# Kernel tuning notes

Hardware: AMD Instinct MI355X
Metric: run time of the kernel (lower is better)

Reference implementation:

```python
import jax, jax.numpy as jnp
import numpy as np

D_MODEL = 1024
D_STATE = 128
HEADDIM = 64
EXPAND = 2
CHUNK = 64
D_CONV = 4
D_INNER = EXPAND * D_MODEL          # 2048
NHEADS = D_INNER // HEADDIM         # 32
D_IN_PROJ = 2 * D_INNER + 2 * D_STATE + NHEADS  # 4384
CONV_CH = D_INNER + 2 * D_STATE     # 2304
EPS = 1e-5


def segsum(x):
    # x: (..., T) -> (..., T, T); out[i, j] = sum_{k=j+1..i} x[k] for i>=j else -inf
    T = x.shape[-1]
    m1 = jnp.tril(jnp.ones((T, T), bool), -1)
    xr = jnp.where(m1, x[..., :, None], 0.0)   # zero above/at diagonal before cumsum
    s = jnp.cumsum(xr, axis=-2)
    m0 = jnp.tril(jnp.ones((T, T), bool), 0)
    return jnp.where(m0, s, -jnp.inf)


def ssd(x, A, B, C, chunk):
    # x: (b, L, h, p); A: (b, L, h); B, C: (b, L, n)  (the h=1 dim of the torch code is squeezed)
    b, L, h, p = x.shape
    c = L // chunk
    x = x.reshape(b, c, chunk, h, p)
    A = A.reshape(b, c, chunk, h).transpose(0, 3, 1, 2)  # (b, h, c, l)
    B = B.reshape(b, c, chunk, -1)                       # (b, c, l, n)
    C = C.reshape(b, c, chunk, -1)
    A_cum = jnp.cumsum(A, axis=-1)                       # (b, h, c, l)
    Lm = jnp.exp(segsum(A))                              # (b, h, c, l, l)
    # intra-chunk (diagonal block) output
    Y_diag = jnp.einsum('bcln,bcsn,bhcls,bcshp->bclhp', C, B, Lm, x)
    # per-chunk states
    decay_states = jnp.exp(A_cum[:, :, :, -1:] - A_cum)  # (b, h, c, l)
    states = jnp.einsum('bcln,bhcl,bclhp->bchpn', B, decay_states, x)
    init = jnp.zeros_like(states[:, :1])
    states = jnp.concatenate([init, states], axis=1)     # (b, c+1, h, p, n)
    # inter-chunk recurrence
    Ac_last = jnp.pad(A_cum[:, :, :, -1], ((0, 0), (0, 0), (1, 0)))  # (b, h, c+1)
    decay_chunk = jnp.exp(segsum(Ac_last))               # (b, h, c+1, c+1)
    new_states = jnp.einsum('bhzc,bchpn->bzhpn', decay_chunk, states)
    states = new_states[:, :-1]                          # (b, c, h, p, n)
    sdo = jnp.exp(A_cum)
    Y_off = jnp.einsum('bcln,bchpn,bhcl->bclhp', C, states, sdo)
    return (Y_diag + Y_off).reshape(b, L, h, p)


def setup_inputs() -> dict:
    key = jax.random.key(0)
    ks = jax.random.split(key, 8)
    return {
        'u': jax.random.normal(ks[0], (2, 4096, D_MODEL), jnp.float32),
        'W_in': jax.random.normal(ks[1], (D_MODEL, D_IN_PROJ), jnp.float32) * 0.02,
        'conv_w': jax.random.normal(ks[2], (CONV_CH, D_CONV), jnp.float32) * 0.3,
        'conv_b': jax.random.normal(ks[3], (CONV_CH,), jnp.float32) * 0.1,
        'dt_bias': jax.random.normal(ks[4], (NHEADS,), jnp.float32),
        'A_log': jax.random.normal(ks[5], (NHEADS,), jnp.float32) * 0.5,
        'D': jax.random.normal(ks[6], (NHEADS,), jnp.float32),
        'norm_w': jnp.ones((D_INNER,), jnp.float32),
        'W_out': jax.random.normal(ks[7], (D_INNER, D_MODEL), jnp.float32) * 0.02,
    }


def reference(u, W_in, conv_w, conv_b, dt_bias, A_log, D, norm_w, W_out):
    b, L, _ = u.shape
    zxbcdt = u @ W_in                                    # (b, L, 4384)
    z = zxbcdt[..., :D_INNER]
    xBC = zxbcdt[..., D_INNER:D_INNER + CONV_CH]
    dt = jax.nn.softplus(zxbcdt[..., -NHEADS:] + dt_bias)  # (b, L, h)
    # depthwise causal conv (Conv1d pad=d_conv-1, truncated to L == left-pad only)
    xc = jnp.pad(xBC.transpose(0, 2, 1), ((0, 0), (0, 0), (D_CONV - 1, 0)))
    xc = jax.lax.conv_general_dilated(
        xc, conv_w[:, None, :], (1,), 'VALID',
        feature_group_count=CONV_CH,
        dimension_numbers=('NCH', 'OIH', 'NCH')) + conv_b[None, :, None]
    xBC = jax.nn.silu(xc.transpose(0, 2, 1))             # (b, L, 2304)
    x = xBC[..., :D_INNER].reshape(b, L, NHEADS, HEADDIM)
    B = xBC[..., D_INNER:D_INNER + D_STATE]
    C = xBC[..., D_INNER + D_STATE:]
    A = -jnp.exp(A_log)                                  # (h,)
    y = ssd(x * dt[..., None], A * dt, B, C, CHUNK)
    y = y + x * D[:, None]
    y = y.reshape(b, L, D_INNER)
    # RMSNorm with gate z
    y = y * jax.nn.silu(z)
    y = y * jax.lax.rsqrt(jnp.mean(y * y, axis=-1, keepdims=True) + EPS) * norm_w
    return y @ W_out
```

## Files before the change

### kernel.cpp

```cpp
#include <hip/hip_runtime.h>
#include <hip/hip_bf16.h>
#include <math.h>

#define D_MODEL   1024
#define D_STATE   128
#define HEADDIM   64
#define CHUNK     64
#define D_INNER   2048
#define NHEADS    32
#define D_IN_PROJ 4384
#define CONV_CH   2304
#define RCOLS     2336
#define WINT_ROWS 4480
#define BATCH     2
#define SEQ       4096
#define NCHUNK    64
#define ROWS      (BATCH*SEQ)
#define EPS_RMS   1e-5f

typedef __hip_bfloat16 bf16;
typedef __bf16 bf16x8_t __attribute__((ext_vector_type(8)));
typedef float  f32x4_t  __attribute__((ext_vector_type(4)));

__device__ __forceinline__ float siluf_(float x){ return x/(1.f+expf(-x)); }
__device__ __forceinline__ void  stf(float* p, float v){ *p = v; }
__device__ __forceinline__ void  stf(bf16* p, float v){ *p = __float2bfloat16(v); }

__device__ __forceinline__ __bf16 tobf(float v){
    __hip_bfloat16 t = __float2bfloat16(v);
    return *reinterpret_cast<__bf16*>(&t);
}
__device__ __forceinline__ unsigned short bfbits(float v){
    __hip_bfloat16 t = __float2bfloat16(v);
    return *reinterpret_cast<unsigned short*>(&t);
}
__device__ __forceinline__ float bfbits2f(unsigned short u){
    union { unsigned u; float f; } cv; cv.u = ((unsigned)u) << 16; return cv.f;
}

__device__ __forceinline__ void async16(const void* g, void* l) {
    __builtin_amdgcn_global_load_lds(
        (const __attribute__((address_space(1))) unsigned int*)g,
        (__attribute__((address_space(3))) unsigned int*)l, 16, 0, 0);
}

struct GemmCore {
    f32x4_t acc[4][4];
    __device__ __forceinline__ void run(const bf16* __restrict__ A, int lda,
                                        const bf16* __restrict__ Bt, int ldb,
                                        int row0, int col0, int k0, int k1,
                                        __bf16* As, __bf16* Bs,
                                        int wave, int lane) {
        const int quad = lane >> 4, l16 = lane & 15;
        const int wr = (wave >> 1) * 64, wc = (wave & 1) * 64;
#pragma unroll
        for (int i = 0; i < 4; ++i)
#pragma unroll
            for (int j = 0; j < 4; ++j) acc[i][j] = (f32x4_t){0.f, 0.f, 0.f, 0.f};
        const int ca0 = wave * 2, ca1 = wave * 2 + 1;
        const int srow = lane >> 2, scol = (lane & 3) * 8;
        const bf16* Ag0 = A  + (size_t)(row0 + ca0 * 16 + srow) * lda + scol;
        const bf16* Ag1 = A  + (size_t)(row0 + ca1 * 16 + srow) * lda + scol;
        const bf16* Bg0 = Bt + (size_t)(col0 + ca0 * 16 + srow) * ldb + scol;
        const bf16* Bg1 = Bt + (size_t)(col0 + ca1 * 16 + srow) * ldb + scol;
        __bf16* Al0 = As + ca0 * 512;
        __bf16* Al1 = As + ca1 * 512;
        __bf16* Bl0 = Bs + ca0 * 512;
        __bf16* Bl1 = Bs + ca1 * 512;
        for (int kk = k0; kk < k1; kk += 32) {
            async16(Ag0 + kk, Al0);
            async16(Ag1 + kk, Al1);
            async16(Bg0 + kk, Bl0);
            async16(Bg1 + kk, Bl1);
            __syncthreads();
            bf16x8_t af[4], bfr[4];
#pragma unroll
            for (int mi = 0; mi < 4; ++mi)
                af[mi] = *(const bf16x8_t*)(As + (wr + mi * 16 + l16) * 32 + quad * 8);
#pragma unroll
            for (int ni = 0; ni < 4; ++ni)
                bfr[ni] = *(const bf16x8_t*)(Bs + (wc + ni * 16 + l16) * 32 + quad * 8);
#pragma unroll
            for (int mi = 0; mi < 4; ++mi)
#pragma unroll
                for (int ni = 0; ni < 4; ++ni)
                    acc[mi][ni] = __builtin_amdgcn_mfma_f32_16x16x32_bf16(
                        af[mi], bfr[ni], acc[mi][ni], 0, 0, 0);
            __syncthreads();
        }
    }
};

__global__ __launch_bounds__(256) void gemm_zr_fused(const bf16* __restrict__ A,
                                                     const bf16* __restrict__ Bt,
                                                     bf16* __restrict__ Z,
                                                     bf16* __restrict__ R) {
    __shared__ __align__(16) __bf16 As[128 * 32];
    __shared__ __align__(16) __bf16 Bs[128 * 32];
    const int tid = threadIdx.x, wave = tid >> 6, lane = tid & 63;
    const int quad = lane >> 4, l16 = lane & 15;
    const int row0 = blockIdx.x * 128;
    const int ct   = blockIdx.y;
    GemmCore g;
    g.run(A, D_MODEL, Bt, D_MODEL, row0, ct * 128, 0, D_MODEL, As, Bs, wave, lane);

    bf16* Cp; int ldc_, cl0, ncols;
    if (ct < 16) { Cp = Z; ldc_ = D_INNER; cl0 = ct * 128;          ncols = D_INNER; }
    else         { Cp = R; ldc_ = RCOLS;   cl0 = ct * 128 - D_INNER; ncols = RCOLS; }
    const int wr = (wave >> 1) * 64, wc = (wave & 1) * 64;
#pragma unroll
    for (int ni = 0; ni < 4; ++ni) {
        int gc = cl0 + wc + ni * 16 + l16;
        if (gc >= ncols) continue;
#pragma unroll
        for (int mi = 0; mi < 4; ++mi)
#pragma unroll
            for (int r = 0; r < 4; ++r) {
                int gr = row0 + wr + mi * 16 + quad * 4 + r;
                stf(&Cp[(size_t)gr * ldc_ + gc], g.acc[mi][ni][r]);
            }
    }
}

__global__ __launch_bounds__(256) void gemm_out_kernel(const bf16* __restrict__ A,
                                                       const bf16* __restrict__ Bt,
                                                       float* __restrict__ out) {
    __shared__ __align__(16) __bf16 As[128 * 32];
    __shared__ __align__(16) __bf16 Bs[128 * 32];
    const int tid = threadIdx.x, wave = tid >> 6, lane = tid & 63;
    const int quad = lane >> 4, l16 = lane & 15;
    const int row0 = blockIdx.x * 128;
    const int col0 = blockIdx.y * 128;
    GemmCore g;
    g.run(A, D_INNER, Bt, D_INNER, row0, col0, 0, D_INNER, As, Bs, wave, lane);
    const int wr = (wave >> 1) * 64, wc = (wave & 1) * 64;
#pragma unroll
    for (int ni = 0; ni < 4; ++ni) {
        int gc = col0 + wc + ni * 16 + l16;
#pragma unroll
        for (int mi = 0; mi < 4; ++mi)
#pragma unroll
            for (int r = 0; r < 4; ++r) {
                int gr = row0 + wr + mi * 16 + quad * 4 + r;
                out[(size_t)gr * D_MODEL + gc] = g.acc[mi][ni][r];
            }
    }
}

__global__ __launch_bounds__(256) void prep_all_kernel(const float* __restrict__ u,
                                                       bf16* __restrict__ u_bf16,
                                                       const float* __restrict__ W_in,
                                                       bf16* __restrict__ W_inT,
                                                       const float* __restrict__ W_out,
                                                       bf16* __restrict__ W_outT,
                                                       const float* __restrict__ conv_w,
                                                       bf16* __restrict__ Wc) {
    __shared__ float tile[32][33];
    int bid = blockIdx.x;
    const int tid = threadIdx.x;

    auto do_transpose = [&](const float* W, bf16* Wt, int R, int C, int c0, int r0) {
        int tx = tid & 31, ty = tid >> 5;
        for (int i = ty; i < 32; i += 8) {
            int r = r0 + i, c = c0 + tx;
            tile[i][tx] = (c < C) ? W[(size_t)r * C + c] : 0.f;
        }
        __syncthreads();
        for (int i = ty; i < 32; i += 8) {
            int c = c0 + i, r = r0 + tx;
            stf(&Wt[(size_t)c * R + r], tile[tx][i]);
        }
    };

    if (bid < 8192) {
        int i = bid * 256 + tid;
        float4 v = ((const float4*)u)[i];
        u_bf16[i * 4 + 0] = __float2bfloat16(v.x);
        u_bf16[i * 4 + 1] = __float2bfloat16(v.y);
        u_bf16[i * 4 + 2] = __float2bfloat16(v.z);
        u_bf16[i * 4 + 3] = __float2bfloat16(v.w);
        return;
    }
    bid -= 8192;
    if (bid < (WINT_ROWS / 32) * (D_MODEL / 32)) {
        int bx = bid % (WINT_ROWS / 32), by = bid / (WINT_ROWS / 32);
        do_transpose(W_in, W_inT, D_MODEL, D_IN_PROJ, bx * 32, by * 32);
        return;
    }
    bid -= (WINT_ROWS / 32) * (D_MODEL / 32);
    if (bid < (D_MODEL / 32) * (D_INNER / 32)) {
        int bx = bid % (D_MODEL / 32), by = bid / (D_MODEL / 32);
        do_transpose(W_out, W_outT, D_INNER, D_MODEL, bx * 32, by * 32);
        return;
    }
    bid -= (D_MODEL / 32) * (D_INNER / 32);
    int i = bid * 256 + tid;
    if (i < CONV_CH * 4) {
        int ch = i >> 2, k = i & 3;
        Wc[k * CONV_CH + ch] = __float2bfloat16(conv_w[ch * 4 + k]);
    }
}

__global__ __launch_bounds__(256) void conv_silu_kernel(const bf16* __restrict__ R,
                                                        const bf16* __restrict__ Wc,
                                                        const float* __restrict__ conv_b,
                                                        bf16* __restrict__ xBC) {
    int idx = blockIdx.x * 256 + threadIdx.x;
    int rq = idx / 288;
    int g = idx - rq * 288;
    int ch0 = g * 8;
    int row0 = rq * 4;
    int l0 = row0 & (SEQ - 1);

    uint4 rv[7];
#pragma unroll
    for (int j = 0; j < 7; ++j) {
        int ls = l0 - 3 + j;
        rv[j] = (ls >= 0) ? *(const uint4*)&R[(size_t)(row0 - 3 + j) * RCOLS + ch0]
                          : make_uint4(0u, 0u, 0u, 0u);
    }
    uint4 wv[4];
#pragma unroll
    for (int k = 0; k < 4; ++k)
        wv[k] = *(const uint4*)&Wc[k * CONV_CH + ch0];
    float4 b0 = ((const float4*)conv_b)[ch0 / 4];
    float4 b1 = ((const float4*)conv_b)[ch0 / 4 + 1];
    const float bias[8] = {b0.x, b0.y, b0.z, b0.w, b1.x, b1.y, b1.z, b1.w};
    float wf[4][8];
#pragma unroll
    for (int k = 0; k < 4; ++k) {
        const unsigned* wp = (const unsigned*)&wv[k];
#pragma unroll
        for (int j2 = 0; j2 < 4; ++j2) {
            wf[k][2 * j2]     = bfbits2f((unsigned short)(wp[j2] & 0xffff));
            wf[k][2 * j2 + 1] = bfbits2f((unsigned short)(wp[j2] >> 16));
        }
    }
#pragma unroll
    for (int j = 0; j < 4; ++j) {
        float acc[8];
#pragma unroll
        for (int cc = 0; cc < 8; ++cc) acc[cc] = bias[cc];
#pragma unroll
        for (int k = 0; k < 4; ++k) {
            const unsigned* vp = (const unsigned*)&rv[j + k];
#pragma unroll
            for (int j2 = 0; j2 < 4; ++j2) {
                unsigned v = vp[j2];
                acc[2 * j2]     += wf[k][2 * j2]     * bfbits2f((unsigned short)(v & 0xffff));
                acc[2 * j2 + 1] += wf[k][2 * j2 + 1] * bfbits2f((unsigned short)(v >> 16));
            }
        }
        unsigned o[4];
#pragma unroll
        for (int j2 = 0; j2 < 4; ++j2)
            o[j2] = (unsigned)bfbits(siluf_(acc[2 * j2])) |
                    ((unsigned)bfbits(siluf_(acc[2 * j2 + 1])) << 16);
        *(uint4*)&xBC[(size_t)(row0 + j) * CONV_CH + ch0] = make_uint4(o[0], o[1], o[2], o[3]);
    }
}

__global__ void dt_kernel(const bf16* __restrict__ R,
                          const float* __restrict__ dt_bias,
                          float* __restrict__ dtb) {
    int i = blockIdx.x * 256 + threadIdx.x;
    int row = i >> 2, h0 = (i & 3) * 8;
    uint4 v = *(const uint4*)&R[(size_t)row * RCOLS + CONV_CH + h0];
    float4 bia0 = ((const float4*)dt_bias)[h0 / 4];
    float4 bia1 = ((const float4*)dt_bias)[h0 / 4 + 1];
    const unsigned vv[4] = {v.x, v.y, v.z, v.w};
    const float bb[8] = {bia0.x, bia0.y, bia0.z, bia0.w, bia1.x, bia1.y, bia1.z, bia1.w};
    float o[8];
#pragma unroll
    for (int j = 0; j < 4; ++j) {
        float a = bfbits2f((unsigned short)(vv[j] & 0xffff)) + bb[2*j];
        float c = bfbits2f((unsigned short)(vv[j] >> 16)) + bb[2*j+1];
        o[2*j]   = (a > 20.f) ? a : log1pf(expf(a));
        o[2*j+1] = (c > 20.f) ? c : log1pf(expf(c));
    }
    float* dp = &dtb[(size_t)row * NHEADS + h0];
    *(float4*)dp       = make_float4(o[0], o[1], o[2], o[3]);
    *(float4*)(dp + 4) = make_float4(o[4], o[5], o[6], o[7]);
}

__global__ void acum_kernel(const float* __restrict__ dtb,
                            const float* __restrict__ A_log,
                            float* __restrict__ Acum,
                            float* __restrict__ decs) {
    int bch = blockIdx.x;
    int h = bch & 31;
    int bc = bch >> 5;
    int c = bc & 63, b = bc >> 6;
    int row0 = b * SEQ + c * CHUNK;
    __shared__ float sh[64];
    int l = threadIdx.x;
    float Ah = -expf(A_log[h]);
    sh[l] = Ah * dtb[(size_t)(row0 + l) * NHEADS + h];
    __syncthreads();
    float s = 0.f;
    for (int j = 0; j <= l; ++j) s += sh[j];
    Acum[(size_t)bch * 64 + l] = s;
    if (l == 63) decs[bch] = expf(s);
}

__global__ __launch_bounds__(256) void states_mfma_kernel(const bf16* __restrict__ xBC,
                                                          const float* __restrict__ dtb,
                                                          const float* __restrict__ Acum,
                                                          bf16* __restrict__ states) {
    __shared__ __align__(16) __bf16 BsT[128 * 72];
    __shared__ __align__(16) __bf16 xdT[4][64 * 72];
    __shared__ float dtdec[4][64];
    int bcq = blockIdx.x;
    int hq = bcq & 7, bc = bcq >> 3;
    int c = bc & 63, b = bc >> 6;
    int tid = threadIdx.x, wave = tid >> 6, lane = tid & 63;
    int h = hq * 4 + wave;
    int bch = bc * 32 + h;
    int row0 = b * SEQ + c * CHUNK;
    int quad = lane >> 4, l16 = lane & 15;

    {
        float alast = Acum[(size_t)bch * 64 + 63];
        float a = Acum[(size_t)bch * 64 + lane];
        dtdec[wave][lane] = dtb[(size_t)(row0 + lane) * NHEADS + h] * expf(alast - a);
    }
    __syncthreads();
    for (int it = 0; it < 8; ++it) {
        int i2 = tid + 256 * it;
        int l0 = (i2 >> 6) * 2;
        int n0 = (i2 & 63) * 2;
        unsigned v0 = *(const unsigned*)&xBC[(size_t)(row0 + l0    ) * CONV_CH + D_INNER + n0];
        unsigned v1 = *(const unsigned*)&xBC[(size_t)(row0 + l0 + 1) * CONV_CH + D_INNER + n0];
        *(unsigned*)&BsT[(n0    ) * 72 + l0] = (v0 & 0xffffu) | (v1 << 16);
        *(unsigned*)&BsT[(n0 + 1) * 72 + l0] = (v0 >> 16) | (v1 & 0xffff0000u);
    }
    for (int it = 0; it < 16; ++it) {
        int l0 = 4 * it + ((lane >> 5) << 1);
        int p0 = (lane & 31) * 2;
        unsigned v0 = *(const unsigned*)&xBC[(size_t)(row0 + l0    ) * CONV_CH + h * 64 + p0];
        unsigned v1 = *(const unsigned*)&xBC[(size_t)(row0 + l0 + 1) * CONV_CH + h * 64 + p0];
        float f0 = dtdec[wave][l0], f1 = dtdec[wave][l0 + 1];
        unsigned w0 = (unsigned)bfbits(bfbits2f((unsigned short)(v0 & 0xffff)) * f0)
                    | ((unsigned)bfbits(bfbits2f((unsigned short)(v1 & 0xffff)) * f1) << 16);
        unsigned w1 = (unsigned)bfbits(bfbits2f((unsigned short)(v0 >> 16)) * f0)
                    | ((unsigned)bfbits(bfbits2f((unsigned short)(v1 >> 16)) * f1) << 16);
        *(unsigned*)&xdT[wave][(p0    ) * 72 + l0] = w0;
        *(unsigned*)&xdT[wave][(p0 + 1) * 72 + l0] = w1;
    }
    __syncthreads();

    f32x4_t acc[4][8];
#pragma unroll
    for (int i = 0; i < 4; ++i)
#pragma unroll
        for (int j = 0; j < 8; ++j) acc[i][j] = (f32x4_t){0.f, 0.f, 0.f, 0.f};
#pragma unroll
    for (int ks = 0; ks < 2; ++ks) {
        bf16x8_t a[4], bb[8];
#pragma unroll
        for (int mi = 0; mi < 4; ++mi)
            a[mi] = *(const bf16x8_t*)(&xdT[wave][(mi * 16 + l16) * 72 + ks * 32 + quad * 8]);
#pragma unroll
        for (int ni = 0; ni < 8; ++ni)
            bb[ni] = *(const bf16x8_t*)(&BsT[(ni * 16 + l16) * 72 + ks * 32 + quad * 8]);
#pragma unroll
        for (int mi = 0; mi < 4; ++mi)
#pragma unroll
            for (int ni = 0; ni < 8; ++ni)
                acc[mi][ni] = __builtin_amdgcn_mfma_f32_16x16x32_bf16(
                    a[mi], bb[ni], acc[mi][ni], 0, 0, 0);
    }
#pragma unroll
    for (int ni = 0; ni < 8; ++ni) {
        int n = ni * 16 + l16;
#pragma unroll
        for (int mi = 0; mi < 4; ++mi)
#pragma unroll
            for (int r = 0; r < 4; ++r) {
                int p = mi * 16 + quad * 4 + r;
                stf(&states[(size_t)bch * 8192 + p * 128 + n], acc[mi][ni][r]);
            }
    }
}

__global__ void scan_kernel(const float* __restrict__ decs,
                            bf16* __restrict__ states) {
    int i = blockIdx.x * 256 + threadIdx.x;
    int pn0 = (i & 2047) * 4;
    int bh = i >> 11;
    int h = bh & 31, b = bh >> 5;
    int bch0 = b * NCHUNK * NHEADS + h;
    const size_t cstride = (size_t)NHEADS * 8192;
    float carry[4] = {0.f, 0.f, 0.f, 0.f};
    bf16* sp = &states[(size_t)bch0 * 8192 + pn0];
    uint2 v = *(const uint2*)sp;
    for (int c = 0; c < NCHUNK; ++c) {
        bf16* spn = sp + ((c + 1 < NCHUNK) ? cstride : 0);
        uint2 vn = *(const uint2*)spn;
        float dec = decs[bch0 + c * NHEADS];
        uint2 o;
        o.x = (unsigned)bfbits(carry[0]) | ((unsigned)bfbits(carry[1]) << 16);
        o.y = (unsigned)bfbits(carry[2]) | ((unsigned)bfbits(carry[3]) << 16);
        *(uint2*)sp = o;
        carry[0] = carry[0] * dec + bfbits2f((unsigned short)(v.x & 0xffff));
        carry[1] = carry[1] * dec + bfbits2f((unsigned short)(v.x >> 16));
        carry[2] = carry[2] * dec + bfbits2f((unsigned short)(v.y & 0xffff));
        carry[3] = carry[3] * dec + bfbits2f((unsigned short)(v.y >> 16));
        sp = spn; v = vn;
    }
}

__global__ __launch_bounds__(64) void y_mfma_kernel(const bf16* __restrict__ xBC,
                                                    const float* __restrict__ dtb,
                                                    const float* __restrict__ Acum,
                                                    const bf16* __restrict__ states,
                                                    const float* __restrict__ Dv,
                                                    bf16* __restrict__ y) {
    __shared__ __align__(16) __bf16 Mm[64 * 72];
    __shared__ __align__(16) __bf16 xsT[64 * 72];
    __shared__ float acs[64], dtss[64], sdos[64];
    int bch = blockIdx.x;
    int h = bch & 31, bc = bch >> 5;
    int c = bc & 63, b = bc >> 6;
    int row0 = b * SEQ + c * CHUNK;
    int lane = threadIdx.x;
    int quad = lane >> 4, l16 = lane & 15;

    {
        float a = Acum[(size_t)bch * 64 + lane];
        acs[lane] = a;
        sdos[lane] = expf(a);
        dtss[lane] = dtb[(size_t)(row0 + lane) * NHEADS + h];
    }
    for (int it = 0; it < 16; ++it) {
        int l0 = 4 * it + ((lane >> 5) << 1);
        int p0 = (lane & 31) * 2;
        unsigned v0 = *(const unsigned*)&xBC[(size_t)(row0 + l0    ) * CONV_CH + h * 64 + p0];
        unsigned v1 = *(const unsigned*)&xBC[(size_t)(row0 + l0 + 1) * CONV_CH + h * 64 + p0];
        *(unsigned*)&xsT[(p0    ) * 72 + l0] = (v0 & 0xffffu) | (v1 << 16);
        *(unsigned*)&xsT[(p0 + 1) * 72 + l0] = (v0 >> 16) | (v1 & 0xffff0000u);
    }
    __syncthreads();

    f32x4_t gacc[4][4];
#pragma unroll
    for (int i = 0; i < 4; ++i)
#pragma unroll
        for (int j = 0; j < 4; ++j) gacc[i][j] = (f32x4_t){0.f, 0.f, 0.f, 0.f};
#pragma unroll
    for (int ks = 0; ks < 4; ++ks) {
        bf16x8_t a[4], bb[4];
#pragma unroll
        for (int mi = 0; mi < 4; ++mi)
            a[mi] = *(const bf16x8_t*)&xBC[(size_t)(row0 + mi * 16 + l16) * CONV_CH +
                                           D_INNER + D_STATE + ks * 32 + quad * 8];
#pragma unroll
        for (int ni = 0; ni < 4; ++ni)
            bb[ni] = *(const bf16x8_t*)&xBC[(size_t)(row0 + ni * 16 + l16) * CONV_CH +
                                            D_INNER + ks * 32 + quad * 8];
#pragma unroll
        for (int mi = 0; mi < 4; ++mi)
#pragma unroll
            for (int ni = 0; ni <= mi; ++ni)
                gacc[mi][ni] = __builtin_amdgcn_mfma_f32_16x16x32_bf16(
                    a[mi], bb[ni], gacc[mi][ni], 0, 0, 0);
    }
#pragma unroll
    for (int ni = 0; ni < 4; ++ni) {
        int s = ni * 16 + l16;
        float ds = dtss[s], as = acs[s];
#pragma unroll
        for (int mi = 0; mi < 4; ++mi)
#pragma unroll
            for (int r = 0; r < 4; ++r) {
                int l = mi * 16 + quad * 4 + r;
                float coef = (s <= l) ? gacc[mi][ni][r] * ds * expf(acs[l] - as) : 0.f;
                Mm[l * 72 + s] = tobf(coef);
            }
    }
    __syncthreads();

    f32x4_t acc[4][4];
#pragma unroll
    for (int i = 0; i < 4; ++i)
#pragma unroll
        for (int j = 0; j < 4; ++j) acc[i][j] = (f32x4_t){0.f, 0.f, 0.f, 0.f};

#pragma unroll
    for (int ks = 0; ks < 2; ++ks) {
        bf16x8_t a[4], bb[4];
#pragma unroll
        for (int mi = 0; mi < 4; ++mi)
            a[mi] = *(const bf16x8_t*)(&Mm[(mi * 16 + l16) * 72 + ks * 32 + quad * 8]);
#pragma unroll
        for (int ni = 0; ni < 4; ++ni)
            bb[ni] = *(const bf16x8_t*)(&xsT[(ni * 16 + l16) * 72 + ks * 32 + quad * 8]);
#pragma unroll
        for (int mi = 0; mi < 4; ++mi)
#pragma unroll
            for (int ni = 0; ni < 4; ++ni)
                acc[mi][ni] = __builtin_amdgcn_mfma_f32_16x16x32_bf16(
                    a[mi], bb[ni], acc[mi][ni], 0, 0, 0);
    }
    float sdo_mi[4];
#pragma unroll
    for (int mi = 0; mi < 4; ++mi) sdo_mi[mi] = sdos[mi * 16 + l16];
#pragma unroll
    for (int ks = 0; ks < 4; ++ks) {
        bf16x8_t a[4], bb[4];
#pragma unroll
        for (int mi = 0; mi < 4; ++mi) {
            const unsigned* cp = (const unsigned*)&xBC[(size_t)(row0 + mi * 16 + l16) * CONV_CH
                                                       + D_INNER + D_STATE + ks * 32 + quad * 8];
            float sc = sdo_mi[mi];
#pragma unroll
            for (int jj = 0; jj < 4; ++jj) {
                unsigned v = cp[jj];
                a[mi][2 * jj    ] = tobf(bfbits2f((unsigned short)(v & 0xffff)) * sc);
                a[mi][2 * jj + 1] = tobf(bfbits2f((unsigned short)(v >> 16)) * sc);
            }
        }
#pragma unroll
        for (int ni = 0; ni < 4; ++ni)
            bb[ni] = *(const bf16x8_t*)&states[(size_t)bch * 8192 + (ni * 16 + l16) * 128
                                               + ks * 32 + quad * 8];
#pragma unroll
        for (int mi = 0; mi < 4; ++mi)
#pragma unroll
            for (int ni = 0; ni < 4; ++ni)
                acc[mi][ni] = __builtin_amdgcn_mfma_f32_16x16x32_bf16(
                    a[mi], bb[ni], acc[mi][ni], 0, 0, 0);
    }
    float Dh = Dv[h];
#pragma unroll
    for (int ni = 0; ni < 4; ++ni) {
        int p = ni * 16 + l16;
#pragma unroll
        for (int mi = 0; mi < 4; ++mi)
#pragma unroll
            for (int r = 0; r < 4; ++r) {
                int l = mi * 16 + quad * 4 + r;
                float xv = bfbits2f(*(const unsigned short*)&xsT[p * 72 + l]);
                stf(&y[(size_t)(row0 + l) * D_INNER + h * 64 + p],
                    acc[mi][ni][r] + Dh * xv);
            }
    }
}

__global__ __launch_bounds__(256) void gate_norm_kernel(const bf16* __restrict__ Z,
                                                        const float* __restrict__ nw,
                                                        bf16* __restrict__ y) {
    int row = blockIdx.x;
    int tid = threadIdx.x;
    int col0 = tid * 8;
    uint4 zv = *(const uint4*)&Z[(size_t)row * D_INNER + col0];
    uint4 yv = *(const uint4*)&y[(size_t)row * D_INNER + col0];
    const unsigned zz[4] = {zv.x, zv.y, zv.z, zv.w};
    const unsigned yy[4] = {yv.x, yv.y, yv.z, yv.w};
    float vals[8];
    float local = 0.f;
#pragma unroll
    for (int j = 0; j < 4; ++j) {
        float z0 = bfbits2f((unsigned short)(zz[j] & 0xffff));
        float z1 = bfbits2f((unsigned short)(zz[j] >> 16));
        float y0 = bfbits2f((unsigned short)(yy[j] & 0xffff));
        float y1 = bfbits2f((unsigned short)(yy[j] >> 16));
        float v0 = y0 * siluf_(z0);
        float v1 = y1 * siluf_(z1);
        vals[2*j] = v0; vals[2*j+1] = v1;
        local += v0 * v0 + v1 * v1;
    }
#pragma unroll
    for (int off = 32; off; off >>= 1) local += __shfl_down(local, off, 64);
    __shared__ float wsum[4];
    if ((tid & 63) == 0) wsum[tid >> 6] = local;
    __syncthreads();
    float total = wsum[0] + wsum[1] + wsum[2] + wsum[3];
    float scale = rsqrtf(total / (float)D_INNER + EPS_RMS);
    float4 w0 = ((const float4*)nw)[col0 / 4];
    float4 w1 = ((const float4*)nw)[col0 / 4 + 1];
    const float ww[8] = {w0.x, w0.y, w0.z, w0.w, w1.x, w1.y, w1.z, w1.w};
    unsigned o[4];
#pragma unroll
    for (int j = 0; j < 4; ++j)
        o[j] = (unsigned)bfbits(vals[2*j] * scale * ww[2*j]) |
               ((unsigned)bfbits(vals[2*j+1] * scale * ww[2*j+1]) << 16);
    *(uint4*)&y[(size_t)row * D_INNER + col0] = make_uint4(o[0], o[1], o[2], o[3]);
}

extern "C" void kernel_launch(void* const* d_in, const int* in_sizes, int n_in,
                              void* d_out, int out_size, void* d_ws, size_t ws_size,
                              hipStream_t stream) {
    const float* u       = (const float*)d_in[0];
    const float* W_in    = (const float*)d_in[1];
    const float* conv_w  = (const float*)d_in[2];
    const float* conv_b  = (const float*)d_in[3];
    const float* dt_bias = (const float*)d_in[4];
    const float* A_log   = (const float*)d_in[5];
    const float* Dv      = (const float*)d_in[6];
    const float* norm_w  = (const float*)d_in[7];
    const float* W_out   = (const float*)d_in[8];
    float* out = (float*)d_out;

    const size_t sz_xBC    = (size_t)ROWS * CONV_CH * 2;
    const size_t sz_Z      = (size_t)ROWS * D_INNER * 2;
    const size_t sz_y      = (size_t)ROWS * D_INNER * 2;
    const size_t sz_states = (size_t)BATCH * NCHUNK * NHEADS * 8192 * 2;
    const size_t sz_dtb    = (size_t)ROWS * NHEADS * 4;
    const size_t sz_Acum   = (size_t)BATCH * NCHUNK * NHEADS * 64 * 4;
    const size_t sz_decs   = (size_t)BATCH * NCHUNK * NHEADS * 4;
    const size_t sz_WinT   = (size_t)WINT_ROWS * D_MODEL * 2;
    const size_t sz_WoutT  = (size_t)D_MODEL * D_INNER * 2;
    const size_t sz_Wc     = (size_t)CONV_CH * 4 * 2;
    const size_t need = sz_xBC + sz_Z + sz_y + sz_states + sz_dtb + sz_Acum +
                        sz_decs + sz_WinT + sz_WoutT + sz_Wc;
    if (ws_size < need) {
        hipMemsetAsync(d_out, 0, (size_t)out_size * sizeof(float), stream);
        return;
    }
    char* ws = (char*)d_ws;
    size_t off = 0;
    bf16*  xBC    = (bf16*) (ws + off); off += sz_xBC;
    bf16*  Z      = (bf16*) (ws + off); off += sz_Z;
    bf16*  y      = (bf16*) (ws + off); off += sz_y;
    bf16*  states = (bf16*) (ws + off); off += sz_states;
    float* dtb    = (float*)(ws + off); off += sz_dtb;
    float* Acum   = (float*)(ws + off); off += sz_Acum;
    float* decs   = (float*)(ws + off); off += sz_decs;
    bf16*  W_inT  = (bf16*) (ws + off); off += sz_WinT;
    bf16*  W_outT = (bf16*) (ws + off); off += sz_WoutT;
    bf16*  Wc     = (bf16*) (ws + off); off += sz_Wc;
    bf16*  R        = states;
    bf16*  u_bf16   = (bf16*)((char*)states + (size_t)ROWS * RCOLS * 2);

    const int prep_blocks = 8192 + (WINT_ROWS / 32) * (D_MODEL / 32)
                          + (D_MODEL / 32) * (D_INNER / 32) + 36;
    prep_all_kernel<<<prep_blocks, 256, 0, stream>>>(
        u, u_bf16, W_in, W_inT, W_out, W_outT, conv_w, Wc);
    gemm_zr_fused<<<dim3(ROWS / 128, 35), 256, 0, stream>>>(u_bf16, W_inT, Z, R);
    conv_silu_kernel<<<ROWS / 4 * 288 / 256, 256, 0, stream>>>(R, Wc, conv_b, xBC);
    dt_kernel<<<ROWS * 4 / 256, 256, 0, stream>>>(R, dt_bias, dtb);
    acum_kernel<<<BATCH * NCHUNK * NHEADS, 64, 0, stream>>>(dtb, A_log, Acum, decs);
    states_mfma_kernel<<<BATCH * NCHUNK * 8, 256, 0, stream>>>(xBC, dtb, Acum, states);
    scan_kernel<<<BATCH * NHEADS * 2048 / 256, 256, 0, stream>>>(decs, states);
    y_mfma_kernel<<<BATCH * NCHUNK * NHEADS, 64, 0, stream>>>(
        xBC, dtb, Acum, states, Dv, y);
    gate_norm_kernel<<<ROWS, 256, 0, stream>>>(Z, norm_w, y);
    gemm_out_kernel<<<dim3(ROWS / 128, D_MODEL / 128), 256, 0, stream>>>(
        y, W_outT, out);
}
```

Before: 411.5 us.

## Fuse conv/dt/acum kernels, split-K output GEMM, deepen scan prefetch

Merges the conv+SiLU, dt softplus and chunk cumsum kernels into a single launch, with the cumsum done as a parallel shared-memory scan over all heads of a chunk. The output GEMM is split along K into two halves that write fp32 partials into reused workspace, followed by a small reduction kernel, to raise block count on the 512-tile grid. The inter-chunk scan now prefetches two chunks ahead. The costs are extra partial-buffer traffic and one more launch for the reduce.

```diff
diff --git a/kernel.cpp b/kernel.cpp
--- a/kernel.cpp
+++ b/kernel.cpp
@@ -122,17 +122,20 @@
     }
 }
 
-__global__ __launch_bounds__(256) void gemm_out_kernel(const bf16* __restrict__ A,
+__global__ __launch_bounds__(256) void gemm_out_splitk(const bf16* __restrict__ A,
                                                        const bf16* __restrict__ Bt,
-                                                       float* __restrict__ out) {
+                                                       float* __restrict__ part) {
     __shared__ __align__(16) __bf16 As[128 * 32];
     __shared__ __align__(16) __bf16 Bs[128 * 32];
     const int tid = threadIdx.x, wave = tid >> 6, lane = tid & 63;
     const int quad = lane >> 4, l16 = lane & 15;
     const int row0 = blockIdx.x * 128;
     const int col0 = blockIdx.y * 128;
+    const int kz   = blockIdx.z;
     GemmCore g;
-    g.run(A, D_INNER, Bt, D_INNER, row0, col0, 0, D_INNER, As, Bs, wave, lane);
+    g.run(A, D_INNER, Bt, D_INNER, row0, col0, kz * 1024, kz * 1024 + 1024,
+          As, Bs, wave, lane);
+    float* P = part + (size_t)kz * ROWS * D_MODEL;
     const int wr = (wave >> 1) * 64, wc = (wave & 1) * 64;
 #pragma unroll
     for (int ni = 0; ni < 4; ++ni) {
@@ -142,9 +145,17 @@
 #pragma unroll
             for (int r = 0; r < 4; ++r) {
                 int gr = row0 + wr + mi * 16 + quad * 4 + r;
-                out[(size_t)gr * D_MODEL + gc] = g.acc[mi][ni][r];
-            }
-    }
+                P[(size_t)gr * D_MODEL + gc] = g.acc[mi][ni][r];
+            }
+    }
+}
+
+__global__ void reduce_out_kernel(const float* __restrict__ part,
+                                  float* __restrict__ out) {
+    int i = blockIdx.x * 256 + threadIdx.x;
+    float4 a = ((const float4*)part)[i];
+    float4 b = ((const float4*)(part + (size_t)ROWS * D_MODEL))[i];
+    ((float4*)out)[i] = make_float4(a.x + b.x, a.y + b.y, a.z + b.z, a.w + b.w);
 }
 
 __global__ __launch_bounds__(256) void prep_all_kernel(const float* __restrict__ u,
@@ -201,106 +212,117 @@
     }
 }
 
-__global__ __launch_bounds__(256) void conv_silu_kernel(const bf16* __restrict__ R,
-                                                        const bf16* __restrict__ Wc,
-                                                        const float* __restrict__ conv_b,
-                                                        bf16* __restrict__ xBC) {
-    int idx = blockIdx.x * 256 + threadIdx.x;
-    int rq = idx / 288;
-    int g = idx - rq * 288;
-    int ch0 = g * 8;
-    int row0 = rq * 4;
-    int l0 = row0 & (SEQ - 1);
-
-    uint4 rv[7];
-#pragma unroll
-    for (int j = 0; j < 7; ++j) {
-        int ls = l0 - 3 + j;
-        rv[j] = (ls >= 0) ? *(const uint4*)&R[(size_t)(row0 - 3 + j) * RCOLS + ch0]
-                          : make_uint4(0u, 0u, 0u, 0u);
-    }
-    uint4 wv[4];
-#pragma unroll
-    for (int k = 0; k < 4; ++k)
-        wv[k] = *(const uint4*)&Wc[k * CONV_CH + ch0];
-    float4 b0 = ((const float4*)conv_b)[ch0 / 4];
-    float4 b1 = ((const float4*)conv_b)[ch0 / 4 + 1];
-    const float bias[8] = {b0.x, b0.y, b0.z, b0.w, b1.x, b1.y, b1.z, b1.w};
-    float wf[4][8];
-#pragma unroll
-    for (int k = 0; k < 4; ++k) {
-        const unsigned* wp = (const unsigned*)&wv[k];
-#pragma unroll
-        for (int j2 = 0; j2 < 4; ++j2) {
-            wf[k][2 * j2]     = bfbits2f((unsigned short)(wp[j2] & 0xffff));
-            wf[k][2 * j2 + 1] = bfbits2f((unsigned short)(wp[j2] >> 16));
-        }
-    }
-#pragma unroll
-    for (int j = 0; j < 4; ++j) {
-        float acc[8];
-#pragma unroll
-        for (int cc = 0; cc < 8; ++cc) acc[cc] = bias[cc];
+#define CONV_BLOCKS 2304
+__global__ __launch_bounds__(256) void conv_dt_kernel(const bf16* __restrict__ R,
+                                                      const bf16* __restrict__ Wc,
+                                                      const float* __restrict__ conv_b,
+                                                      const float* __restrict__ dt_bias,
+                                                      const float* __restrict__ A_log,
+                                                      bf16* __restrict__ xBC,
+                                                      float* __restrict__ dtb,
+                                                      float* __restrict__ Acum,
+                                                      float* __restrict__ decs) {
+    __shared__ float sh[32][65];
+    const int tid = threadIdx.x;
+    if (blockIdx.x < CONV_BLOCKS) {
+        int idx = blockIdx.x * 256 + tid;
+        int rq = idx / 288;
+        int g = idx - rq * 288;
+        int ch0 = g * 8;
+        int row0 = rq * 4;
+        int l0 = row0 & (SEQ - 1);
+
+        uint4 rv[7];
+#pragma unroll
+        for (int j = 0; j < 7; ++j) {
+            int ls = l0 - 3 + j;
+            rv[j] = (ls >= 0) ? *(const uint4*)&R[(size_t)(row0 - 3 + j) * RCOLS + ch0]
+                              : make_uint4(0u, 0u, 0u, 0u);
+        }
+        uint4 wv[4];
+#pragma unroll
+        for (int k = 0; k < 4; ++k)
+            wv[k] = *(const uint4*)&Wc[k * CONV_CH + ch0];
+        float4 b0 = ((const float4*)conv_b)[ch0 / 4];
+        float4 b1 = ((const float4*)conv_b)[ch0 / 4 + 1];
+        const float bias[8] = {b0.x, b0.y, b0.z, b0.w, b1.x, b1.y, b1.z, b1.w};
+        float wf[4][8];
 #pragma unroll
         for (int k = 0; k < 4; ++k) {
-            const unsigned* vp = (const unsigned*)&rv[j + k];
+            const unsigned* wp = (const unsigned*)&wv[k];
 #pragma unroll
             for (int j2 = 0; j2 < 4; ++j2) {
-                unsigned v = vp[j2];
-                acc[2 * j2]     += wf[k][2 * j2]     * bfbits2f((unsigned short)(v & 0xffff));
-                acc[2 * j2 + 1] += wf[k][2 * j2 + 1] * bfbits2f((unsigned short)(v >> 16));
-            }
-        }
-        unsigned o[4];
-#pragma unroll
-        for (int j2 = 0; j2 < 4; ++j2)
-            o[j2] = (unsigned)bfbits(siluf_(acc[2 * j2])) |
-                    ((unsigned)bfbits(siluf_(acc[2 * j2 + 1])) << 16);
-        *(uint4*)&xBC[(size_t)(row0 + j) * CONV_CH + ch0] = make_uint4(o[0], o[1], o[2], o[3]);
-    }
-}
-
-__global__ void dt_kernel(const bf16* __restrict__ R,
-                          const float* __restrict__ dt_bias,
-                          float* __restrict__ dtb) {
-    int i = blockIdx.x * 256 + threadIdx.x;
-    int row = i >> 2, h0 = (i & 3) * 8;
-    uint4 v = *(const uint4*)&R[(size_t)row * RCOLS + CONV_CH + h0];
-    float4 bia0 = ((const float4*)dt_bias)[h0 / 4];
-    float4 bia1 = ((const float4*)dt_bias)[h0 / 4 + 1];
-    const unsigned vv[4] = {v.x, v.y, v.z, v.w};
-    const float bb[8] = {bia0.x, bia0.y, bia0.z, bia0.w, bia1.x, bia1.y, bia1.z, bia1.w};
-    float o[8];
-#pragma unroll
-    for (int j = 0; j < 4; ++j) {
-        float a = bfbits2f((unsigned short)(vv[j] & 0xffff)) + bb[2*j];
-        float c = bfbits2f((unsigned short)(vv[j] >> 16)) + bb[2*j+1];
-        o[2*j]   = (a > 20.f) ? a : log1pf(expf(a));
-        o[2*j+1] = (c > 20.f) ? c : log1pf(expf(c));
-    }
-    float* dp = &dtb[(size_t)row * NHEADS + h0];
-    *(float4*)dp       = make_float4(o[0], o[1], o[2], o[3]);
-    *(float4*)(dp + 4) = make_float4(o[4], o[5], o[6], o[7]);
-}
-
-__global__ void acum_kernel(const float* __restrict__ dtb,
-                            const float* __restrict__ A_log,
-                            float* __restrict__ Acum,
-                            float* __restrict__ decs) {
-    int bch = blockIdx.x;
-    int h = bch & 31;
-    int bc = bch >> 5;
-    int c = bc & 63, b = bc >> 6;
-    int row0 = b * SEQ + c * CHUNK;
-    __shared__ float sh[64];
-    int l = threadIdx.x;
-    float Ah = -expf(A_log[h]);
-    sh[l] = Ah * dtb[(size_t)(row0 + l) * NHEADS + h];
+                wf[k][2 * j2]     = bfbits2f((unsigned short)(wp[j2] & 0xffff));
+                wf[k][2 * j2 + 1] = bfbits2f((unsigned short)(wp[j2] >> 16));
+            }
+        }
+#pragma unroll
+        for (int j = 0; j < 4; ++j) {
+            float acc[8];
+#pragma unroll
+            for (int cc = 0; cc < 8; ++cc) acc[cc] = bias[cc];
+#pragma unroll
+            for (int k = 0; k < 4; ++k) {
+                const unsigned* vp = (const unsigned*)&rv[j + k];
+#pragma unroll
+                for (int j2 = 0; j2 < 4; ++j2) {
+                    unsigned v = vp[j2];
+                    acc[2 * j2]     += wf[k][2 * j2]     * bfbits2f((unsigned short)(v & 0xffff));
+                    acc[2 * j2 + 1] += wf[k][2 * j2 + 1] * bfbits2f((unsigned short)(v >> 16));
+                }
+            }
+            unsigned o[4];
+#pragma unroll
+            for (int j2 = 0; j2 < 4; ++j2)
+                o[j2] = (unsigned)bfbits(siluf_(acc[2 * j2])) |
+                        ((unsigned)bfbits(siluf_(acc[2 * j2 + 1])) << 16);
+            *(uint4*)&xBC[(size_t)(row0 + j) * CONV_CH + ch0] = make_uint4(o[0], o[1], o[2], o[3]);
+        }
+        return;
+    }
+    int bc = blockIdx.x - CONV_BLOCKS;
+    int row0 = bc * CHUNK;
+    {
+        int l = tid >> 2, h0 = (tid & 3) * 8;
+        uint4 v = *(const uint4*)&R[(size_t)(row0 + l) * RCOLS + CONV_CH + h0];
+        float4 bia0 = ((const float4*)dt_bias)[h0 / 4];
+        float4 bia1 = ((const float4*)dt_bias)[h0 / 4 + 1];
+        const unsigned vv[4] = {v.x, v.y, v.z, v.w};
+        const float bb[8] = {bia0.x, bia0.y, bia0.z, bia0.w,
+                             bia1.x, bia1.y, bia1.z, bia1.w};
+        float o[8];
+#pragma unroll
+        for (int j = 0; j < 4; ++j) {
+            float a = bfbits2f((unsigned short)(vv[j] & 0xffff)) + bb[2*j];
+            float c2 = bfbits2f((unsigned short)(vv[j] >> 16)) + bb[2*j+1];
+            o[2*j]   = (a  > 20.f) ? a  : log1pf(expf(a));
+            o[2*j+1] = (c2 > 20.f) ? c2 : log1pf(expf(c2));
+        }
+        float* dp = &dtb[(size_t)(row0 + l) * NHEADS + h0];
+        *(float4*)dp       = make_float4(o[0], o[1], o[2], o[3]);
+        *(float4*)(dp + 4) = make_float4(o[4], o[5], o[6], o[7]);
+#pragma unroll
+        for (int j = 0; j < 8; ++j)
+            sh[h0 + j][l] = o[j] * (-expf(A_log[h0 + j]));
+    }
     __syncthreads();
-    float s = 0.f;
-    for (int j = 0; j <= l; ++j) s += sh[j];
-    Acum[(size_t)bch * 64 + l] = s;
-    if (l == 63) decs[bch] = expf(s);
+    int h = tid >> 3, l0 = (tid & 7) * 8;
+    for (int d = 1; d < 64; d <<= 1) {
+        float add[8];
+#pragma unroll
+        for (int j = 0; j < 8; ++j) {
+            int l = l0 + j;
+            add[j] = (l >= d) ? sh[h][l - d] : 0.f;
+        }
+        __syncthreads();
+#pragma unroll
+        for (int j = 0; j < 8; ++j) sh[h][l0 + j] += add[j];
+        __syncthreads();
+    }
+    float* Ap = &Acum[(size_t)(bc * 32 + h) * 64 + l0];
+#pragma unroll
+    for (int j = 0; j < 8; ++j) Ap[j] = sh[h][l0 + j];
+    if (l0 == 56) decs[bc * 32 + h] = expf(sh[h][63]);
 }
 
 __global__ __launch_bounds__(256) void states_mfma_kernel(const bf16* __restrict__ xBC,
@@ -392,21 +414,23 @@
     int bch0 = b * NCHUNK * NHEADS + h;
     const size_t cstride = (size_t)NHEADS * 8192;
     float carry[4] = {0.f, 0.f, 0.f, 0.f};
-    bf16* sp = &states[(size_t)bch0 * 8192 + pn0];
-    uint2 v = *(const uint2*)sp;
+    bf16* sp0 = &states[(size_t)bch0 * 8192 + pn0];
+    bf16* sp = sp0;
+    uint2 v0 = *(const uint2*)sp0;
+    uint2 v1 = *(const uint2*)(sp0 + cstride);
     for (int c = 0; c < NCHUNK; ++c) {
-        bf16* spn = sp + ((c + 1 < NCHUNK) ? cstride : 0);
-        uint2 vn = *(const uint2*)spn;
+        int cn = (c + 2 < NCHUNK) ? c + 2 : NCHUNK - 1;
+        uint2 vn = *(const uint2*)(sp0 + (size_t)cn * cstride);
         float dec = decs[bch0 + c * NHEADS];
         uint2 o;
         o.x = (unsigned)bfbits(carry[0]) | ((unsigned)bfbits(carry[1]) << 16);
         o.y = (unsigned)bfbits(carry[2]) | ((unsigned)bfbits(carry[3]) << 16);
         *(uint2*)sp = o;
-        carry[0] = carry[0] * dec + bfbits2f((unsigned short)(v.x & 0xffff));
-        carry[1] = carry[1] * dec + bfbits2f((unsigned short)(v.x >> 16));
-        carry[2] = carry[2] * dec + bfbits2f((unsigned short)(v.y & 0xffff));
-        carry[3] = carry[3] * dec + bfbits2f((unsigned short)(v.y >> 16));
-        sp = spn; v = vn;
+        carry[0] = carry[0] * dec + bfbits2f((unsigned short)(v0.x & 0xffff));
+        carry[1] = carry[1] * dec + bfbits2f((unsigned short)(v0.x >> 16));
+        carry[2] = carry[2] * dec + bfbits2f((unsigned short)(v0.y & 0xffff));
+        carry[3] = carry[3] * dec + bfbits2f((unsigned short)(v0.y >> 16));
+        sp += cstride; v0 = v1; v1 = vn;
     }
 }
 
@@ -632,20 +656,21 @@
     bf16*  Wc     = (bf16*) (ws + off); off += sz_Wc;
     bf16*  R        = states;
     bf16*  u_bf16   = (bf16*)((char*)states + (size_t)ROWS * RCOLS * 2);
+    float* out_part = (float*)states;
 
     const int prep_blocks = 8192 + (WINT_ROWS / 32) * (D_MODEL / 32)
                           + (D_MODEL / 32) * (D_INNER / 32) + 36;
     prep_all_kernel<<<prep_blocks, 256, 0, stream>>>(
         u, u_bf16, W_in, W_inT, W_out, W_outT, conv_w, Wc);
     gemm_zr_fused<<<dim3(ROWS / 128, 35), 256, 0, stream>>>(u_bf16, W_inT, Z, R);
-    conv_silu_kernel<<<ROWS / 4 * 288 / 256, 256, 0, stream>>>(R, Wc, conv_b, xBC);
-    dt_kernel<<<ROWS * 4 / 256, 256, 0, stream>>>(R, dt_bias, dtb);
-    acum_kernel<<<BATCH * NCHUNK * NHEADS, 64, 0, stream>>>(dtb, A_log, Acum, decs);
+    conv_dt_kernel<<<CONV_BLOCKS + BATCH * NCHUNK, 256, 0, stream>>>(
+        R, Wc, conv_b, dt_bias, A_log, xBC, dtb, Acum, decs);
     states_mfma_kernel<<<BATCH * NCHUNK * 8, 256, 0, stream>>>(xBC, dtb, Acum, states);
     scan_kernel<<<BATCH * NHEADS * 2048 / 256, 256, 0, stream>>>(decs, states);
     y_mfma_kernel<<<BATCH * NCHUNK * NHEADS, 64, 0, stream>>>(
         xBC, dtb, Acum, states, Dv, y);
     gate_norm_kernel<<<ROWS, 256, 0, stream>>>(Z, norm_w, y);
-    gemm_out_kernel<<<dim3(ROWS / 128, D_MODEL / 128), 256, 0, stream>>>(
-        y, W_outT, out);
-}
+    gemm_out_splitk<<<dim3(ROWS / 128, D_MODEL / 128, 2), 256, 0, stream>>>(
+        y, W_outT, out_part);
+    reduce_out_kernel<<<ROWS * D_MODEL / 4 / 256, 256, 0, stream>>>(out_part, out);
+}
```

Measured after the change: 421.4 us. 2.4% more time.
